# Kernel optimization log

Measured on AMD Instinct MI355X. Metric: run time of the kernel, lower is better.

Reference implementation:

```python
import jax, jax.numpy as jnp
import numpy as np

STEPS = 8         # Euler integration steps (module arg `steps`)
ALPHA = 1e-2      # membrane (Laplacian) weight of the Riemannian metric
GAMMA = 1e-3      # absolute displacement weight (keeps metric invertible)


def _l_hat(spatial, dtype):
    """Fourier transfer function of L = gamma + alpha * (-discrete Laplacian).

    Circulant boundary conditions -> diagonal in Fourier space.
    Returns array broadcastable over the spatial dims, shape == spatial.
    """
    nd = len(spatial)
    lap = None
    for i, n in enumerate(spatial):
        k = jnp.arange(n, dtype=dtype)
        t = 2.0 - 2.0 * jnp.cos(2.0 * jnp.pi * k / n)
        shape = [1] * nd
        shape[i] = n
        t = t.reshape(shape)
        lap = t if lap is None else lap + t
    return GAMMA + ALPHA * lap


def _pullback(f, disp, grid):
    """Sample f at x + disp(x) with trilinear interpolation, wrap boundary.

    f:    [B, C, X, Y, Z]  field to pull back
    disp: [B, D, X, Y, Z]  voxel displacement (D == number of spatial dims)
    grid: [D, X, Y, Z]     identity coordinate grid
    """
    coords = grid[None] + disp  # [B, D, X, Y, Z]
    nd = grid.shape[0]

    def samp(channel, co):  # channel: [X,Y,Z], co: [D,X,Y,Z]
        return jax.scipy.ndimage.map_coordinates(
            channel, [co[d] for d in range(nd)], order=1, mode='wrap')

    # vmap over batch, then over channels (coords shared across channels)
    return jax.vmap(lambda fb, cb: jax.vmap(lambda ch: samp(ch, cb))(fb))(f, coords)


def _shoot(v):
    """Geodesic shooting of initial velocity v: [B, D, *spatial] -> phi (disp).

    m0 = L v0 (momentum); each Euler step: v = K m, compose phi with dt*v,
    transport momentum by pullback (fast scheme, no Jacobian correction).
    """
    spatial = v.shape[2:]
    axes = tuple(range(-len(spatial), 0))
    lh = _l_hat(spatial, v.dtype)

    def L(x):
        return jnp.fft.ifftn(jnp.fft.fftn(x, axes=axes) * lh, axes=axes).real.astype(v.dtype)

    def K(x):
        return jnp.fft.ifftn(jnp.fft.fftn(x, axes=axes) / lh, axes=axes).real.astype(v.dtype)

    grid = jnp.stack(jnp.meshgrid(
        *[jnp.arange(n, dtype=v.dtype) for n in spatial], indexing='ij'))  # [D, X, Y, Z]

    dt = 1.0 / STEPS
    m0 = L(v)
    phi0 = jnp.zeros_like(v)

    def step(carry, _):
        phi, m = carry
        sv = dt * K(m)                        # small velocity for this step
        phi = _pullback(phi, sv, grid) + sv   # phi <- phi o (id + dt*v)
        m = _pullback(m, sv, grid)            # fast momentum transport
        return (phi, m), None

    (phi, _), _ = jax.lax.scan(step, (phi0, m0), None, length=STEPS)
    return phi


def setup_inputs() -> dict:
    key = jax.random.key(0)
    v = 0.5 * jax.random.normal(key, (2, 3, 128, 128, 128), dtype=jnp.float32)
    return {"v": v}


def reference(v) -> jnp.ndarray:
    # Module does movedim(1,-1) -> shoot -> movedim(-1,1); we keep the
    # channels-first layout throughout, which is mathematically identical.
    return _shoot(v)
```

## Files before the change

### kernel.cpp

```cpp
#include <hip/hip_runtime.h>
#include <math.h>

#define NN 128
#define VV (NN*NN*NN)

#define K_GAMMA 1e-3f
#define K_ALPHA 1e-2f
#define K_DTN3  5.9604644775390625e-08f
#define K_W0    0.04908738521234052f

__device__ __forceinline__ void fft128_fwd(float* re, float* im, const int stride,
                                           const int lane,
                                           const float* __restrict__ twr,
                                           const float* __restrict__ twi) {
#pragma unroll
  for (int lh = 6; lh >= 0; --lh) {
    __syncthreads();
    const int h  = 1 << lh;
    const int j  = lane & (h - 1);
    const int i0 = ((lane - j) << 1) + j;
    const int i1 = i0 + h;
    const int tw = j << (6 - lh);
    const float wr = twr[tw], ws = twi[tw];
    const int a = i0 * stride, b = i1 * stride;
    const float ar = re[a], ai = im[a];
    const float br = re[b], bi = im[b];
    re[a] = ar + br;
    im[a] = ai + bi;
    const float dr = ar - br, di = ai - bi;
    re[b] = dr * wr + di * ws;
    im[b] = di * wr - dr * ws;
  }
  __syncthreads();
}

__device__ __forceinline__ void fft128_inv(float* re, float* im, const int stride,
                                           const int lane,
                                           const float* __restrict__ twr,
                                           const float* __restrict__ twi) {
#pragma unroll
  for (int lh = 0; lh <= 6; ++lh) {
    __syncthreads();
    const int h  = 1 << lh;
    const int j  = lane & (h - 1);
    const int i0 = ((lane - j) << 1) + j;
    const int i1 = i0 + h;
    const int tw = j << (6 - lh);
    const float wr = twr[tw], ws = twi[tw];
    const int a = i0 * stride, b = i1 * stride;
    const float ar = re[a], ai = im[a];
    const float br = re[b], bi = im[b];
    const float cr = br * wr - bi * ws;
    const float ci = br * ws + bi * wr;
    re[a] = ar + cr;
    im[a] = ai + ci;
    re[b] = ar - cr;
    im[b] = ai - ci;
  }
  __syncthreads();
}

__device__ __forceinline__ void make_twiddles(int tid, float* twr, float* twi) {
  if (tid < 64) {
    float s, c;
    sincosf((float)tid * K_W0, &s, &c);
    twr[tid] = c;
    twi[tid] = s;
  }
}

__global__ __launch_bounds__(256) void k_stencil_L(const float* __restrict__ v,
                                                   float* __restrict__ m) {
  const int idx = blockIdx.x * 256 + threadIdx.x;
  const int vox = idx & (VV - 1);
  const int r   = idx >> 21;
  const int z = vox & 127, y = (vox >> 7) & 127, x = vox >> 14;
  const float* base = v + (size_t)r * VV;
  const float c = base[vox];
  const int xm = (x - 1) & 127, xp = (x + 1) & 127;
  const int ym = (y - 1) & 127, yp = (y + 1) & 127;
  const int zm = (z - 1) & 127, zp = (z + 1) & 127;
  const float nsum = base[(xm << 14) | (y << 7) | z] + base[(xp << 14) | (y << 7) | z]
                   + base[(x << 14) | (ym << 7) | z] + base[(x << 14) | (yp << 7) | z]
                   + base[(x << 14) | (y << 7) | zm] + base[(x << 14) | (y << 7) | zp];
  m[idx] = K_GAMMA * c + K_ALPHA * (6.0f * c - nsum);
}

__global__ __launch_bounds__(256) void k_fft_z_fwd(const float* __restrict__ m,
                                                   float2* __restrict__ cbuf) {
  __shared__ float twr[64], twi[64];
  __shared__ float re[4][128], im[4][128];
  const int tid = threadIdx.x, lane = tid & 63, w = tid >> 6;
  make_twiddles(tid, twr, twi);
  const int line = blockIdx.x * 4 + w;
  const int p = line >> 14;
  const float* r0 = m + (size_t)(2 * p) * VV + (size_t)(line & 16383) * 128;
  const float* r1 = r0 + VV;
  re[w][lane] = r0[lane];  re[w][lane + 64] = r0[lane + 64];
  im[w][lane] = r1[lane];  im[w][lane + 64] = r1[lane + 64];
  fft128_fwd(re[w], im[w], 1, lane, twr, twi);
  float2* dst = cbuf + (size_t)line * 128;
  dst[lane]      = make_float2(re[w][lane],      im[w][lane]);
  dst[lane + 64] = make_float2(re[w][lane + 64], im[w][lane + 64]);
}

template <bool INV>
__global__ __launch_bounds__(512) void k_fft_y(float2* __restrict__ cbuf) {
  __shared__ float twr[64], twi[64];
  __shared__ float re[128 * 9], im[128 * 9];
  const int tid = threadIdx.x, lane = tid & 63, wv = tid >> 6;
  make_twiddles(tid, twr, twi);
  const int bid = blockIdx.x;
  const int p = bid >> 11, rem = bid & 2047;
  const int x = rem >> 4, z0 = (rem & 15) << 3;
  float2* base = cbuf + (size_t)p * VV + (size_t)x * 16384 + z0;
  {
    int e = tid;       int y = e >> 3, zz = e & 7;
    float2 val = base[y * 128 + zz];
    re[y * 9 + zz] = val.x;  im[y * 9 + zz] = val.y;
    e = tid + 512;     y = e >> 3; zz = e & 7;
    val = base[y * 128 + zz];
    re[y * 9 + zz] = val.x;  im[y * 9 + zz] = val.y;
  }
  if (INV) fft128_inv(re + wv, im + wv, 9, lane, twr, twi);
  else     fft128_fwd(re + wv, im + wv, 9, lane, twr, twi);
  {
    int e = tid;       int y = e >> 3, zz = e & 7;
    base[y * 128 + zz] = make_float2(re[y * 9 + zz], im[y * 9 + zz]);
    e = tid + 512;     y = e >> 3; zz = e & 7;
    base[y * 128 + zz] = make_float2(re[y * 9 + zz], im[y * 9 + zz]);
  }
}

__global__ __launch_bounds__(512) void k_fft_x_fused(float2* __restrict__ cbuf) {
  __shared__ float twr[64], twi[64], tt[128];
  __shared__ float re[128 * 9], im[128 * 9];
  const int tid = threadIdx.x, lane = tid & 63, wv = tid >> 6;
  make_twiddles(tid, twr, twi);
  if (tid < 128) {
    const int br = (int)(__brev((unsigned)tid) >> 25);
    tt[tid] = 2.0f - 2.0f * cosf((float)br * K_W0);
  }
  const int bid = blockIdx.x;
  const int p = bid >> 11, rem = bid & 2047;
  const int y = rem >> 4, z0 = (rem & 15) << 3;
  float2* base = cbuf + (size_t)p * VV + (size_t)y * 128 + z0;
  {
    int e = tid;       int xx = e >> 3, zz = e & 7;
    float2 val = base[(size_t)xx * 16384 + zz];
    re[xx * 9 + zz] = val.x;  im[xx * 9 + zz] = val.y;
    e = tid + 512;     xx = e >> 3; zz = e & 7;
    val = base[(size_t)xx * 16384 + zz];
    re[xx * 9 + zz] = val.x;  im[xx * 9 + zz] = val.y;
  }
  fft128_fwd(re + wv, im + wv, 9, lane, twr, twi);
  {
    const float tyv = tt[y];
    const float tzv = tt[z0 + wv];
#pragma unroll
    for (int i = lane; i < 128; i += 64) {
      const float sc = K_DTN3 / (K_GAMMA + K_ALPHA * (tt[i] + tyv + tzv));
      re[i * 9 + wv] *= sc;
      im[i * 9 + wv] *= sc;
    }
  }
  fft128_inv(re + wv, im + wv, 9, lane, twr, twi);
  {
    int e = tid;       int xx = e >> 3, zz = e & 7;
    base[(size_t)xx * 16384 + zz] = make_float2(re[xx * 9 + zz], im[xx * 9 + zz]);
    e = tid + 512;     xx = e >> 3; zz = e & 7;
    base[(size_t)xx * 16384 + zz] = make_float2(re[xx * 9 + zz], im[xx * 9 + zz]);
  }
}

__global__ __launch_bounds__(256) void k_fft_z_inv(float2* __restrict__ cbuf) {
  __shared__ float twr[64], twi[64];
  __shared__ float re[4][128], im[4][128];
  const int tid = threadIdx.x, lane = tid & 63, w = tid >> 6;
  make_twiddles(tid, twr, twi);
  const int line = blockIdx.x * 4 + w;
  float2* src = cbuf + (size_t)line * 128;
  float2 v0 = src[lane], v1 = src[lane + 64];
  re[w][lane] = v0.x;  im[w][lane] = v0.y;
  re[w][lane + 64] = v1.x;  im[w][lane + 64] = v1.y;
  fft128_inv(re[w], im[w], 1, lane, twr, twi);
  src[lane]      = make_float2(re[w][lane],      im[w][lane]);
  src[lane + 64] = make_float2(re[w][lane + 64], im[w][lane + 64]);
}

__global__ __launch_bounds__(256) void k_pullback(const float* __restrict__ svc,
                                                  const float* __restrict__ phiA,
                                                  const float* __restrict__ mA,
                                                  float* __restrict__ phiB,
                                                  float* __restrict__ mB) {
  const int idx = blockIdx.x * 256 + threadIdx.x;
  const int b   = idx >> 21;
  const int vox = idx & (VV - 1);
  const int z = vox & 127, y = (vox >> 7) & 127, x = vox >> 14;
  const int r0 = b * 3;
  const float d0 = svc[(size_t)((r0)     >> 1) * 2 * VV + ((size_t)vox << 1) + ((r0)     & 1)];
  const float d1 = svc[(size_t)((r0 + 1) >> 1) * 2 * VV + ((size_t)vox << 1) + ((r0 + 1) & 1)];
  const float d2 = svc[(size_t)((r0 + 2) >> 1) * 2 * VV + ((size_t)vox << 1) + ((r0 + 2) & 1)];
  const float cx = (float)x + d0, cy = (float)y + d1, cz = (float)z + d2;
  const float flx = floorf(cx), fly = floorf(cy), flz = floorf(cz);
  const float wx = cx - flx, wy = cy - fly, wz = cz - flz;
  const int x0 = ((int)flx) & 127, y0 = ((int)fly) & 127, z0 = ((int)flz) & 127;
  const int x1 = (x0 + 1) & 127,  y1 = (y0 + 1) & 127,  z1 = (z0 + 1) & 127;
  const int o000 = (x0 * 128 + y0) * 128 + z0;
  const int o001 = (x0 * 128 + y0) * 128 + z1;
  const int o010 = (x0 * 128 + y1) * 128 + z0;
  const int o011 = (x0 * 128 + y1) * 128 + z1;
  const int o100 = (x1 * 128 + y0) * 128 + z0;
  const int o101 = (x1 * 128 + y0) * 128 + z1;
  const int o110 = (x1 * 128 + y1) * 128 + z0;
  const int o111 = (x1 * 128 + y1) * 128 + z1;
  const float w000 = (1.f - wx) * (1.f - wy) * (1.f - wz);
  const float w001 = (1.f - wx) * (1.f - wy) * wz;
  const float w010 = (1.f - wx) * wy * (1.f - wz);
  const float w011 = (1.f - wx) * wy * wz;
  const float w100 = wx * (1.f - wy) * (1.f - wz);
  const float w101 = wx * (1.f - wy) * wz;
  const float w110 = wx * wy * (1.f - wz);
  const float w111 = wx * wy * wz;
  const size_t sb = (size_t)b * 3 * VV;
  const float dd[3] = {d0, d1, d2};
#pragma unroll
  for (int c = 0; c < 3; ++c) {
    const size_t vb = sb + (size_t)c * VV;
    const float* P = phiA + vb;
    const float gp = w000 * P[o000] + w001 * P[o001] + w010 * P[o010] + w011 * P[o011]
                   + w100 * P[o100] + w101 * P[o101] + w110 * P[o110] + w111 * P[o111];
    phiB[vb + vox] = gp + dd[c];
    const float* M = mA + vb;
    const float gm = w000 * M[o000] + w001 * M[o001] + w010 * M[o010] + w011 * M[o011]
                   + w100 * M[o100] + w101 * M[o101] + w110 * M[o110] + w111 * M[o111];
    mB[vb + vox] = gm;
  }
}

extern "C" void kernel_launch(void* const* d_in, const int* in_sizes, int n_in,
                              void* d_out, int out_size, void* d_ws, size_t ws_size,
                              hipStream_t stream) {
  (void)in_sizes; (void)n_in; (void)out_size; (void)ws_size;
  const float* v = (const float*)d_in[0];
  float* phi0 = (float*)d_out;
  float* ws   = (float*)d_ws;
  const size_t FV = (size_t)6 * VV;
  float* phi1 = ws;
  float* mA   = ws + FV;
  float* mB   = ws + 2 * FV;
  float2* cbuf = (float2*)(ws + 3 * FV);

  hipMemsetAsync(phi0, 0, FV * sizeof(float), stream);
  k_stencil_L<<<dim3((unsigned)(FV / 256)), dim3(256), 0, stream>>>(v, mA);

  float* phiA = phi0; float* phiB = phi1;
  float* ma = mA;     float* mb = mB;
  for (int s = 0; s < 8; ++s) {
    k_fft_z_fwd<<<dim3(12288), dim3(256), 0, stream>>>(ma, cbuf);
    k_fft_y<false><<<dim3(6144), dim3(512), 0, stream>>>(cbuf);
    k_fft_x_fused<<<dim3(6144), dim3(512), 0, stream>>>(cbuf);
    k_fft_y<true><<<dim3(6144), dim3(512), 0, stream>>>(cbuf);
    k_fft_z_inv<<<dim3(12288), dim3(256), 0, stream>>>(cbuf);
    k_pullback<<<dim3(16384), dim3(256), 0, stream>>>((const float*)cbuf, phiA, ma, phiB, mb);
    float* t = phiA; phiA = phiB; phiB = t;
    t = ma; ma = mb; mb = t;
  }
}
```

Measured before the change: 2.551 ms.

## Fuse z/y FFT passes into plane kernels, widen x tiles, pair voxels in pullback

Merges the separate z and y FFT kernels into a single kernel per direction. That kernel loads a whole 128x128 plane into padded shared memory (about 132KB) and does both 1D transforms before writing back, which removes two full round trips of the complex buffer through global memory per step. The x-axis FFT kernel now processes 16 z-columns per block instead of 8, and the pullback kernel handles two adjacent voxels per thread using float4 loads of the interleaved velocity buffer and float2 stores. The trade-off is that the plane kernel runs only 384 blocks, each using very large shared memory with 1024 threads, which limits occupancy and parallelism.

Result: slower. 2.699 ms (+5.8%).

```diff
diff --git a/kernel.cpp b/kernel.cpp
--- a/kernel.cpp
+++ b/kernel.cpp
@@ -1,72 +1,49 @@
 #include <hip/hip_runtime.h>
 #include <math.h>
 
-#define NN 128
-#define VV (NN*NN*NN)
+#define VV (128*128*128)
 
 #define K_GAMMA 1e-3f
 #define K_ALPHA 1e-2f
 #define K_DTN3  5.9604644775390625e-08f
 #define K_W0    0.04908738521234052f
 
-__device__ __forceinline__ void fft128_fwd(float* re, float* im, const int stride,
-                                           const int lane,
-                                           const float* __restrict__ twr,
-                                           const float* __restrict__ twi) {
-#pragma unroll
-  for (int lh = 6; lh >= 0; --lh) {
-    __syncthreads();
-    const int h  = 1 << lh;
-    const int j  = lane & (h - 1);
-    const int i0 = ((lane - j) << 1) + j;
-    const int i1 = i0 + h;
-    const int tw = j << (6 - lh);
-    const float wr = twr[tw], ws = twi[tw];
-    const int a = i0 * stride, b = i1 * stride;
-    const float ar = re[a], ai = im[a];
-    const float br = re[b], bi = im[b];
-    re[a] = ar + br;
-    im[a] = ai + bi;
-    const float dr = ar - br, di = ai - bi;
-    re[b] = dr * wr + di * ws;
-    im[b] = di * wr - dr * ws;
-  }
-  __syncthreads();
-}
-
-__device__ __forceinline__ void fft128_inv(float* re, float* im, const int stride,
-                                           const int lane,
-                                           const float* __restrict__ twr,
-                                           const float* __restrict__ twi) {
-#pragma unroll
-  for (int lh = 0; lh <= 6; ++lh) {
-    __syncthreads();
-    const int h  = 1 << lh;
-    const int j  = lane & (h - 1);
-    const int i0 = ((lane - j) << 1) + j;
-    const int i1 = i0 + h;
-    const int tw = j << (6 - lh);
-    const float wr = twr[tw], ws = twi[tw];
-    const int a = i0 * stride, b = i1 * stride;
-    const float ar = re[a], ai = im[a];
-    const float br = re[b], bi = im[b];
-    const float cr = br * wr - bi * ws;
-    const float ci = br * ws + bi * wr;
-    re[a] = ar + cr;
-    im[a] = ai + ci;
-    re[b] = ar - cr;
-    im[b] = ai - ci;
-  }
-  __syncthreads();
-}
-
-__device__ __forceinline__ void make_twiddles(int tid, float* twr, float* twi) {
-  if (tid < 64) {
-    float s, c;
-    sincosf((float)tid * K_W0, &s, &c);
-    twr[tid] = c;
-    twi[tid] = s;
-  }
+__device__ __forceinline__ void bf_fwd(float* re, float* im, const int stride,
+                                       const int lane, const int lh,
+                                       const float* __restrict__ twr,
+                                       const float* __restrict__ twi) {
+  const int h  = 1 << lh;
+  const int j  = lane & (h - 1);
+  const int i0 = ((lane - j) << 1) + j;
+  const int i1 = i0 + h;
+  const int tw = j << (6 - lh);
+  const float wr = twr[tw], ws = twi[tw];
+  const int a = i0 * stride, b = i1 * stride;
+  const float ar = re[a], ai = im[a];
+  const float br = re[b], bi = im[b];
+  re[a] = ar + br;  im[a] = ai + bi;
+  const float dr = ar - br, di = ai - bi;
+  re[b] = dr * wr + di * ws;
+  im[b] = di * wr - dr * ws;
+}
+
+__device__ __forceinline__ void bf_inv(float* re, float* im, const int stride,
+                                       const int lane, const int lh,
+                                       const float* __restrict__ twr,
+                                       const float* __restrict__ twi) {
+  const int h  = 1 << lh;
+  const int j  = lane & (h - 1);
+  const int i0 = ((lane - j) << 1) + j;
+  const int i1 = i0 + h;
+  const int tw = j << (6 - lh);
+  const float wr = twr[tw], ws = twi[tw];
+  const int a = i0 * stride, b = i1 * stride;
+  const float ar = re[a], ai = im[a];
+  const float br = re[b], bi = im[b];
+  const float cr = br * wr - bi * ws;
+  const float ci = br * ws + bi * wr;
+  re[a] = ar + cr;  im[a] = ai + ci;
+  re[b] = ar - cr;  im[b] = ai - ci;
 }
 
 __global__ __launch_bounds__(256) void k_stencil_L(const float* __restrict__ v,
@@ -86,155 +63,201 @@
   m[idx] = K_GAMMA * c + K_ALPHA * (6.0f * c - nsum);
 }
 
-__global__ __launch_bounds__(256) void k_fft_z_fwd(const float* __restrict__ m,
-                                                   float2* __restrict__ cbuf) {
+template <bool INV>
+__global__ __launch_bounds__(1024) void k_fft_zy(const float* __restrict__ m,
+                                                 float2* __restrict__ cbuf) {
   __shared__ float twr[64], twi[64];
-  __shared__ float re[4][128], im[4][128];
-  const int tid = threadIdx.x, lane = tid & 63, w = tid >> 6;
-  make_twiddles(tid, twr, twi);
-  const int line = blockIdx.x * 4 + w;
-  const int p = line >> 14;
-  const float* r0 = m + (size_t)(2 * p) * VV + (size_t)(line & 16383) * 128;
-  const float* r1 = r0 + VV;
-  re[w][lane] = r0[lane];  re[w][lane + 64] = r0[lane + 64];
-  im[w][lane] = r1[lane];  im[w][lane + 64] = r1[lane + 64];
-  fft128_fwd(re[w], im[w], 1, lane, twr, twi);
-  float2* dst = cbuf + (size_t)line * 128;
-  dst[lane]      = make_float2(re[w][lane],      im[w][lane]);
-  dst[lane + 64] = make_float2(re[w][lane + 64], im[w][lane + 64]);
-}
-
-template <bool INV>
-__global__ __launch_bounds__(512) void k_fft_y(float2* __restrict__ cbuf) {
-  __shared__ float twr[64], twi[64];
-  __shared__ float re[128 * 9], im[128 * 9];
+  __shared__ float re[128 * 129], im[128 * 129];
   const int tid = threadIdx.x, lane = tid & 63, wv = tid >> 6;
-  make_twiddles(tid, twr, twi);
-  const int bid = blockIdx.x;
-  const int p = bid >> 11, rem = bid & 2047;
-  const int x = rem >> 4, z0 = (rem & 15) << 3;
-  float2* base = cbuf + (size_t)p * VV + (size_t)x * 16384 + z0;
-  {
-    int e = tid;       int y = e >> 3, zz = e & 7;
-    float2 val = base[y * 128 + zz];
-    re[y * 9 + zz] = val.x;  im[y * 9 + zz] = val.y;
-    e = tid + 512;     y = e >> 3; zz = e & 7;
-    val = base[y * 128 + zz];
-    re[y * 9 + zz] = val.x;  im[y * 9 + zz] = val.y;
-  }
-  if (INV) fft128_inv(re + wv, im + wv, 9, lane, twr, twi);
-  else     fft128_fwd(re + wv, im + wv, 9, lane, twr, twi);
-  {
-    int e = tid;       int y = e >> 3, zz = e & 7;
-    base[y * 128 + zz] = make_float2(re[y * 9 + zz], im[y * 9 + zz]);
-    e = tid + 512;     y = e >> 3; zz = e & 7;
-    base[y * 128 + zz] = make_float2(re[y * 9 + zz], im[y * 9 + zz]);
+  if (tid < 64) {
+    float s, c; sincosf((float)tid * K_W0, &s, &c);
+    twr[tid] = c; twi[tid] = s;
+  }
+  const int p = blockIdx.x >> 7, x = blockIdx.x & 127;
+  float2* cb = cbuf + (size_t)p * VV + (size_t)x * 16384;
+  if (!INV) {
+    const float* r0 = m + (size_t)(2 * p) * VV + (size_t)x * 16384;
+    const float* r1 = r0 + VV;
+#pragma unroll
+    for (int i = 0; i < 16; ++i) {
+      const int e = tid + i * 1024, y = e >> 7, z = e & 127;
+      re[y * 129 + z] = r0[e];  im[y * 129 + z] = r1[e];
+    }
+  } else {
+#pragma unroll
+    for (int i = 0; i < 16; ++i) {
+      const int e = tid + i * 1024, y = e >> 7, z = e & 127;
+      const float2 v = cb[e];
+      re[y * 129 + z] = v.x;  im[y * 129 + z] = v.y;
+    }
+  }
+  if (!INV) {
+    for (int lh = 6; lh >= 0; --lh) {
+      __syncthreads();
+#pragma unroll
+      for (int l = 0; l < 8; ++l) {
+        const int y = (wv << 3) | l;
+        bf_fwd(re + y * 129, im + y * 129, 1, lane, lh, twr, twi);
+      }
+    }
+    for (int lh = 6; lh >= 0; --lh) {
+      __syncthreads();
+#pragma unroll
+      for (int l = 0; l < 8; ++l) {
+        const int z = (wv << 3) | l;
+        bf_fwd(re + z, im + z, 129, lane, lh, twr, twi);
+      }
+    }
+  } else {
+    for (int lh = 0; lh <= 6; ++lh) {
+      __syncthreads();
+#pragma unroll
+      for (int l = 0; l < 8; ++l) {
+        const int z = (wv << 3) | l;
+        bf_inv(re + z, im + z, 129, lane, lh, twr, twi);
+      }
+    }
+    for (int lh = 0; lh <= 6; ++lh) {
+      __syncthreads();
+#pragma unroll
+      for (int l = 0; l < 8; ++l) {
+        const int y = (wv << 3) | l;
+        bf_inv(re + y * 129, im + y * 129, 1, lane, lh, twr, twi);
+      }
+    }
+  }
+  __syncthreads();
+#pragma unroll
+  for (int i = 0; i < 16; ++i) {
+    const int e = tid + i * 1024, y = e >> 7, z = e & 127;
+    cb[e] = make_float2(re[y * 129 + z], im[y * 129 + z]);
   }
 }
 
 __global__ __launch_bounds__(512) void k_fft_x_fused(float2* __restrict__ cbuf) {
   __shared__ float twr[64], twi[64], tt[128];
-  __shared__ float re[128 * 9], im[128 * 9];
+  __shared__ float re[128 * 17], im[128 * 17];
   const int tid = threadIdx.x, lane = tid & 63, wv = tid >> 6;
-  make_twiddles(tid, twr, twi);
+  if (tid < 64) {
+    float s, c; sincosf((float)tid * K_W0, &s, &c);
+    twr[tid] = c; twi[tid] = s;
+  }
   if (tid < 128) {
     const int br = (int)(__brev((unsigned)tid) >> 25);
     tt[tid] = 2.0f - 2.0f * cosf((float)br * K_W0);
   }
   const int bid = blockIdx.x;
-  const int p = bid >> 11, rem = bid & 2047;
-  const int y = rem >> 4, z0 = (rem & 15) << 3;
-  float2* base = cbuf + (size_t)p * VV + (size_t)y * 128 + z0;
-  {
-    int e = tid;       int xx = e >> 3, zz = e & 7;
-    float2 val = base[(size_t)xx * 16384 + zz];
-    re[xx * 9 + zz] = val.x;  im[xx * 9 + zz] = val.y;
-    e = tid + 512;     xx = e >> 3; zz = e & 7;
-    val = base[(size_t)xx * 16384 + zz];
-    re[xx * 9 + zz] = val.x;  im[xx * 9 + zz] = val.y;
-  }
-  fft128_fwd(re + wv, im + wv, 9, lane, twr, twi);
+  const int p = bid >> 10, rem = bid & 1023;
+  const int y = rem >> 3, z0 = (rem & 7) << 4;
+  float2* base = cbuf + (size_t)p * VV + (size_t)(y * 128 + z0);
+#pragma unroll
+  for (int i = 0; i < 4; ++i) {
+    const int e = tid + i * 512, xx = e >> 4, zz = e & 15;
+    const float2 v = base[(size_t)xx * 16384 + zz];
+    re[xx * 17 + zz] = v.x;  im[xx * 17 + zz] = v.y;
+  }
+  for (int lh = 6; lh >= 0; --lh) {
+    __syncthreads();
+#pragma unroll
+    for (int l = 0; l < 2; ++l) {
+      const int zz = wv + (l << 3);
+      bf_fwd(re + zz, im + zz, 17, lane, lh, twr, twi);
+    }
+  }
+  __syncthreads();
   {
     const float tyv = tt[y];
-    const float tzv = tt[z0 + wv];
-#pragma unroll
-    for (int i = lane; i < 128; i += 64) {
-      const float sc = K_DTN3 / (K_GAMMA + K_ALPHA * (tt[i] + tyv + tzv));
-      re[i * 9 + wv] *= sc;
-      im[i * 9 + wv] *= sc;
-    }
-  }
-  fft128_inv(re + wv, im + wv, 9, lane, twr, twi);
-  {
-    int e = tid;       int xx = e >> 3, zz = e & 7;
-    base[(size_t)xx * 16384 + zz] = make_float2(re[xx * 9 + zz], im[xx * 9 + zz]);
-    e = tid + 512;     xx = e >> 3; zz = e & 7;
-    base[(size_t)xx * 16384 + zz] = make_float2(re[xx * 9 + zz], im[xx * 9 + zz]);
-  }
-}
-
-__global__ __launch_bounds__(256) void k_fft_z_inv(float2* __restrict__ cbuf) {
-  __shared__ float twr[64], twi[64];
-  __shared__ float re[4][128], im[4][128];
-  const int tid = threadIdx.x, lane = tid & 63, w = tid >> 6;
-  make_twiddles(tid, twr, twi);
-  const int line = blockIdx.x * 4 + w;
-  float2* src = cbuf + (size_t)line * 128;
-  float2 v0 = src[lane], v1 = src[lane + 64];
-  re[w][lane] = v0.x;  im[w][lane] = v0.y;
-  re[w][lane + 64] = v1.x;  im[w][lane + 64] = v1.y;
-  fft128_inv(re[w], im[w], 1, lane, twr, twi);
-  src[lane]      = make_float2(re[w][lane],      im[w][lane]);
-  src[lane + 64] = make_float2(re[w][lane + 64], im[w][lane + 64]);
-}
-
-__global__ __launch_bounds__(256) void k_pullback(const float* __restrict__ svc,
+#pragma unroll
+    for (int l = 0; l < 2; ++l) {
+      const int zz = wv + (l << 3);
+      const float tzv = tt[z0 + zz];
+#pragma unroll
+      for (int i = lane; i < 128; i += 64) {
+        const float sc = K_DTN3 / (K_GAMMA + K_ALPHA * (tt[i] + tyv + tzv));
+        re[i * 17 + zz] *= sc;
+        im[i * 17 + zz] *= sc;
+      }
+    }
+  }
+  for (int lh = 0; lh <= 6; ++lh) {
+    __syncthreads();
+#pragma unroll
+    for (int l = 0; l < 2; ++l) {
+      const int zz = wv + (l << 3);
+      bf_inv(re + zz, im + zz, 17, lane, lh, twr, twi);
+    }
+  }
+  __syncthreads();
+#pragma unroll
+  for (int i = 0; i < 4; ++i) {
+    const int e = tid + i * 512, xx = e >> 4, zz = e & 15;
+    base[(size_t)xx * 16384 + zz] = make_float2(re[xx * 17 + zz], im[xx * 17 + zz]);
+  }
+}
+
+struct Corner { int o[8]; float w[8]; };
+
+__device__ __forceinline__ Corner mk_corner(float cx, float cy, float cz) {
+  Corner c;
+  const float flx = floorf(cx), fly = floorf(cy), flz = floorf(cz);
+  const float wx = cx - flx, wy = cy - fly, wz = cz - flz;
+  const int x0 = ((int)flx) & 127, y0 = ((int)fly) & 127, z0 = ((int)flz) & 127;
+  const int x1 = (x0 + 1) & 127,  y1 = (y0 + 1) & 127,  z1 = (z0 + 1) & 127;
+  c.o[0] = (x0 * 128 + y0) * 128 + z0;  c.o[1] = (x0 * 128 + y0) * 128 + z1;
+  c.o[2] = (x0 * 128 + y1) * 128 + z0;  c.o[3] = (x0 * 128 + y1) * 128 + z1;
+  c.o[4] = (x1 * 128 + y0) * 128 + z0;  c.o[5] = (x1 * 128 + y0) * 128 + z1;
+  c.o[6] = (x1 * 128 + y1) * 128 + z0;  c.o[7] = (x1 * 128 + y1) * 128 + z1;
+  const float ux = 1.f - wx, uy = 1.f - wy, uz = 1.f - wz;
+  c.w[0] = ux * uy * uz;  c.w[1] = ux * uy * wz;
+  c.w[2] = ux * wy * uz;  c.w[3] = ux * wy * wz;
+  c.w[4] = wx * uy * uz;  c.w[5] = wx * uy * wz;
+  c.w[6] = wx * wy * uz;  c.w[7] = wx * wy * wz;
+  return c;
+}
+
+__device__ __forceinline__ float tri8(const float* __restrict__ V, const Corner& c) {
+  float s = 0.f;
+#pragma unroll
+  for (int k = 0; k < 8; ++k) s += c.w[k] * V[c.o[k]];
+  return s;
+}
+
+__global__ __launch_bounds__(256) void k_pullback(const float4* __restrict__ sv4,
                                                   const float* __restrict__ phiA,
                                                   const float* __restrict__ mA,
                                                   float* __restrict__ phiB,
                                                   float* __restrict__ mB) {
   const int idx = blockIdx.x * 256 + threadIdx.x;
-  const int b   = idx >> 21;
-  const int vox = idx & (VV - 1);
+  const int b   = idx >> 20;
+  const int pr  = idx & ((VV >> 1) - 1);
+  const int vox = pr << 1;
   const int z = vox & 127, y = (vox >> 7) & 127, x = vox >> 14;
-  const int r0 = b * 3;
-  const float d0 = svc[(size_t)((r0)     >> 1) * 2 * VV + ((size_t)vox << 1) + ((r0)     & 1)];
-  const float d1 = svc[(size_t)((r0 + 1) >> 1) * 2 * VV + ((size_t)vox << 1) + ((r0 + 1) & 1)];
-  const float d2 = svc[(size_t)((r0 + 2) >> 1) * 2 * VV + ((size_t)vox << 1) + ((r0 + 2) & 1)];
-  const float cx = (float)x + d0, cy = (float)y + d1, cz = (float)z + d2;
-  const float flx = floorf(cx), fly = floorf(cy), flz = floorf(cz);
-  const float wx = cx - flx, wy = cy - fly, wz = cz - flz;
-  const int x0 = ((int)flx) & 127, y0 = ((int)fly) & 127, z0 = ((int)flz) & 127;
-  const int x1 = (x0 + 1) & 127,  y1 = (y0 + 1) & 127,  z1 = (z0 + 1) & 127;
-  const int o000 = (x0 * 128 + y0) * 128 + z0;
-  const int o001 = (x0 * 128 + y0) * 128 + z1;
-  const int o010 = (x0 * 128 + y1) * 128 + z0;
-  const int o011 = (x0 * 128 + y1) * 128 + z1;
-  const int o100 = (x1 * 128 + y0) * 128 + z0;
-  const int o101 = (x1 * 128 + y0) * 128 + z1;
-  const int o110 = (x1 * 128 + y1) * 128 + z0;
-  const int o111 = (x1 * 128 + y1) * 128 + z1;
-  const float w000 = (1.f - wx) * (1.f - wy) * (1.f - wz);
-  const float w001 = (1.f - wx) * (1.f - wy) * wz;
-  const float w010 = (1.f - wx) * wy * (1.f - wz);
-  const float w011 = (1.f - wx) * wy * wz;
-  const float w100 = wx * (1.f - wy) * (1.f - wz);
-  const float w101 = wx * (1.f - wy) * wz;
-  const float w110 = wx * wy * (1.f - wz);
-  const float w111 = wx * wy * wz;
+  float d0A, d1A, d2A, d0B, d1B, d2B;
+  if (b == 0) {
+    const float4 f0 = sv4[pr];
+    const float4 f1 = sv4[(VV >> 1) + pr];
+    d0A = f0.x; d1A = f0.y; d0B = f0.z; d1B = f0.w;
+    d2A = f1.x; d2B = f1.z;
+  } else {
+    const float4 f1 = sv4[(VV >> 1) + pr];
+    const float4 f2 = sv4[2 * (VV >> 1) + pr];
+    d0A = f1.y; d0B = f1.w;
+    d1A = f2.x; d2A = f2.y; d1B = f2.z; d2B = f2.w;
+  }
+  const Corner cA = mk_corner((float)x + d0A, (float)y + d1A, (float)z + d2A);
+  const Corner cB = mk_corner((float)x + d0B, (float)y + d1B, (float)(z + 1) + d2B);
+  const float ddA[3] = {d0A, d1A, d2A};
+  const float ddB[3] = {d0B, d1B, d2B};
   const size_t sb = (size_t)b * 3 * VV;
-  const float dd[3] = {d0, d1, d2};
 #pragma unroll
   for (int c = 0; c < 3; ++c) {
     const size_t vb = sb + (size_t)c * VV;
     const float* P = phiA + vb;
-    const float gp = w000 * P[o000] + w001 * P[o001] + w010 * P[o010] + w011 * P[o011]
-                   + w100 * P[o100] + w101 * P[o101] + w110 * P[o110] + w111 * P[o111];
-    phiB[vb + vox] = gp + dd[c];
+    const float gpA = tri8(P, cA), gpB = tri8(P, cB);
+    *(float2*)(phiB + vb + vox) = make_float2(gpA + ddA[c], gpB + ddB[c]);
     const float* M = mA + vb;
-    const float gm = w000 * M[o000] + w001 * M[o001] + w010 * M[o010] + w011 * M[o011]
-                   + w100 * M[o100] + w101 * M[o101] + w110 * M[o110] + w111 * M[o111];
-    mB[vb + vox] = gm;
+    const float gmA = tri8(M, cA), gmB = tri8(M, cB);
+    *(float2*)(mB + vb + vox) = make_float2(gmA, gmB);
   }
 }
 
@@ -257,12 +280,11 @@
   float* phiA = phi0; float* phiB = phi1;
   float* ma = mA;     float* mb = mB;
   for (int s = 0; s < 8; ++s) {
-    k_fft_z_fwd<<<dim3(12288), dim3(256), 0, stream>>>(ma, cbuf);
-    k_fft_y<false><<<dim3(6144), dim3(512), 0, stream>>>(cbuf);
-    k_fft_x_fused<<<dim3(6144), dim3(512), 0, stream>>>(cbuf);
-    k_fft_y<true><<<dim3(6144), dim3(512), 0, stream>>>(cbuf);
-    k_fft_z_inv<<<dim3(12288), dim3(256), 0, stream>>>(cbuf);
-    k_pullback<<<dim3(16384), dim3(256), 0, stream>>>((const float*)cbuf, phiA, ma, phiB, mb);
+    k_fft_zy<false><<<dim3(384), dim3(1024), 0, stream>>>(ma, cbuf);
+    k_fft_x_fused<<<dim3(3072), dim3(512), 0, stream>>>(cbuf);
+    k_fft_zy<true><<<dim3(384), dim3(1024), 0, stream>>>(ma, cbuf);
+    k_pullback<<<dim3(VV / 256), dim3(256), 0, stream>>>((const float4*)cbuf,
+                                                         phiA, ma, phiB, mb);
     float* t = phiA; phiA = phiB; phiB = t;
     t = ma; ma = mb; mb = t;
   }
```
